# Performance work log

Hardware: AMD Instinct MI355X
Metric: run time of the kernel (lower is better)

## Reference

```python
import jax, jax.numpy as jnp
import numpy as np

N_SEQ, SEQ_LEN, HIDDEN, BATCH = 2048, 128, 128, 64


def setup_inputs() -> dict:
    key = jax.random.key(0)
    ks = jax.random.split(key, 6)
    s_ih = 1.0 / np.sqrt(SEQ_LEN)
    s_hh = 1.0 / np.sqrt(HIDDEN)
    s_fc = 1.0 / np.sqrt(N_SEQ * HIDDEN)
    return {
        "x": jax.random.normal(ks[0], (BATCH, N_SEQ, SEQ_LEN), dtype=jnp.float32),
        "h0": jnp.zeros((BATCH, HIDDEN), dtype=jnp.float32),
        "c0": jnp.zeros((BATCH, HIDDEN), dtype=jnp.float32),
        # LSTM weights, PyTorch gate order (i, f, g, o) packed on last axis
        "W_ih": jax.random.uniform(ks[1], (SEQ_LEN, 4 * HIDDEN), jnp.float32, -s_ih, s_ih),
        "W_hh": jax.random.uniform(ks[2], (HIDDEN, 4 * HIDDEN), jnp.float32, -s_hh, s_hh),
        "b": jax.random.uniform(ks[3], (4 * HIDDEN,), jnp.float32, -s_ih, s_ih),
        "fc_w": jax.random.uniform(ks[4], (2, N_SEQ * HIDDEN), jnp.float32, -s_fc, s_fc),
        "fc_b": jax.random.uniform(ks[5], (2,), jnp.float32, -s_fc, s_fc),
    }


def _lstm(x_tmajor, h0, c0, W_ih, W_hh, b):
    # x_tmajor: [T, B, D]. Precompute input projection in one big matmul.
    pre = jnp.einsum("tbd,dg->tbg", x_tmajor, W_ih) + b  # [T, B, 4H]
    H = h0.shape[-1]

    def step(carry, pre_t):
        h, c = carry
        gates = pre_t + h @ W_hh  # [B, 4H]
        i = jax.nn.sigmoid(gates[:, 0 * H:1 * H])
        f = jax.nn.sigmoid(gates[:, 1 * H:2 * H])
        g = jnp.tanh(gates[:, 2 * H:3 * H])
        o = jax.nn.sigmoid(gates[:, 3 * H:4 * H])
        c_new = f * c + i * g
        h_new = o * jnp.tanh(c_new)
        return (h_new, c_new), h_new

    (_, _), hs = jax.lax.scan(step, (h0, c0), pre)
    return hs  # [T, B, H]


def reference(x, h0, c0, W_ih, W_hh, b, fc_w, fc_b):
    xt = jnp.transpose(x, (1, 0, 2))              # [T, B, D]
    hs = _lstm(xt, h0, c0, W_ih, W_hh, b)          # [T, B, H]
    hb = jnp.transpose(hs, (1, 0, 2))              # [B, T, H]
    flat = hb.reshape(hb.shape[0], -1)             # [B, T*H]
    return flat @ fc_w.T + fc_b                    # [B, 2]
```

## Files before the change

### kernel.cpp

```cpp
#include <hip/hip_runtime.h>

#define T_SEQ 2048
#define NBATCH 64
#define DIM 128
#define HID 128
#define G4 512
#define GRP 16
#define TT 8
#define LOG2E 1.44269504088896f

typedef _Float16 h2v   __attribute__((ext_vector_type(2)));
typedef _Float16 f16x8 __attribute__((ext_vector_type(8)));
typedef float    f32x4 __attribute__((ext_vector_type(4)));

__device__ __forceinline__ unsigned pack2(float lo, float hi) {
    h2v v; v.x = (_Float16)lo; v.y = (_Float16)hi;
    return __builtin_bit_cast(unsigned, v);
}
__device__ __forceinline__ float dot2(unsigned a, unsigned b, float c) {
#if __has_builtin(__builtin_amdgcn_fdot2)
    return __builtin_amdgcn_fdot2(__builtin_bit_cast(h2v, a),
                                  __builtin_bit_cast(h2v, b), c, false);
#else
    h2v av = __builtin_bit_cast(h2v, a), bv = __builtin_bit_cast(h2v, b);
    c = fmaf((float)av.x, (float)bv.x, c);
    return fmaf((float)av.y, (float)bv.y, c);
#endif
}
__device__ __forceinline__ float rcp_(float x)  { return __builtin_amdgcn_rcpf(x); }
__device__ __forceinline__ float exp2_(float x) { return __builtin_amdgcn_exp2f(x); }
template <int CTRL>
__device__ __forceinline__ float qmov(float v) {
    int r = __builtin_amdgcn_mov_dpp(__builtin_bit_cast(int, v), CTRL, 0xF, 0xF, true);
    return __builtin_bit_cast(float, r);
}
#define QP_XOR1 0xB1
#define QP_XOR2 0x4E
#define QP_B0   0x00
#define QP_B1   0x55
#define QP_B2   0xAA
#define QP_B3   0xFF

__device__ __forceinline__ void barrier_lgkm() {
    asm volatile("s_waitcnt lgkmcnt(0)\n\ts_barrier" ::: "memory");
    __builtin_amdgcn_sched_barrier(0);
}

__global__ __launch_bounds__(256) void prep(
    const float* __restrict__ x, _Float16* __restrict__ x16)
{
    const size_t gtid   = (size_t)blockIdx.x * blockDim.x + threadIdx.x;
    const size_t stride = (size_t)gridDim.x * blockDim.x;
    const size_t n_x2 = (size_t)NBATCH * T_SEQ * DIM / 2;
    for (size_t i = gtid; i < n_x2; i += stride) {
        float2 v = reinterpret_cast<const float2*>(x)[i];
        h2v p; p.x = (_Float16)v.x; p.y = (_Float16)v.y;
        reinterpret_cast<h2v*>(x16)[i] = p;
    }
}

__global__ __launch_bounds__(512, 2) void pre_mfma(
    const _Float16* __restrict__ x16,
    const float* __restrict__ Wih,
    const float* __restrict__ bias,
    _Float16* __restrict__ pre,
    int t0)
{
    const int tid = threadIdx.x;
    const int w   = tid >> 6;
    const int l   = tid & 63;
    const int col = l & 15;
    const int hi  = l >> 4;
    const int bg  = blockIdx.x & 3;
    const int lt0 = (blockIdx.x >> 2) * TT;
    const int batch = bg * 16 + col;

    f16x8 aX[4][4];
    f32x4 bv[4];
    #pragma unroll
    for (int j = 0; j < 4; ++j) {
        const int chr  = 16 * (4 * w + j) + col;
        const int wcol = (chr & 3) * HID + (chr >> 2);
        const float sc = ((chr & 3) == 2) ? -2.0f * LOG2E : -LOG2E;
        #pragma unroll
        for (int ks = 0; ks < 4; ++ks) {
            f16x8 a;
            #pragma unroll
            for (int i = 0; i < 8; ++i) {
                int k = ks * 32 + hi * 8 + i;
                a[i] = (_Float16)(Wih[(size_t)k * G4 + wcol] * sc);
            }
            aX[j][ks] = a;
        }
        #pragma unroll
        for (int r = 0; r < 4; ++r) {
            const int ch = 16 * (4 * w + j) + 4 * hi + r;
            const float scr = ((ch & 3) == 2) ? -2.0f * LOG2E : -LOG2E;
            bv[j][r] = bias[(ch & 3) * HID + (ch >> 2)] * scr;
        }
    }

    const _Float16* xb_base = x16 + (size_t)batch * T_SEQ * DIM + hi * 8;

    for (int tt = 0; tt < TT; ++tt) {
        const int lt = lt0 + tt;
        const int t  = t0 + lt;
        f16x8 xf[4];
        #pragma unroll
        for (int ks = 0; ks < 4; ++ks)
            xf[ks] = *reinterpret_cast<const f16x8*>(
                xb_base + (size_t)t * DIM + ks * 32);
        #pragma unroll
        for (int j = 0; j < 4; ++j) {
            f32x4 acc = bv[j];
            #pragma unroll
            for (int ks = 0; ks < 4; ++ks)
                acc = __builtin_amdgcn_mfma_f32_16x16x32_f16(aX[j][ks], xf[ks], acc, 0, 0, 0);
            uint2 o;
            o.x = pack2(acc[0], acc[1]);
            o.y = pack2(acc[2], acc[3]);
            *reinterpret_cast<uint2*>(
                pre + ((size_t)lt * NBATCH + batch) * G4 + 16 * (4 * w + j) + 4 * hi) = o;
        }
    }
}

__global__ __launch_bounds__(512, 1) void lstm_scan(
    const _Float16* __restrict__ pre,
    const float* __restrict__ Whh,
    const float* __restrict__ h0,
    const float* __restrict__ c0,
    float* __restrict__ state,
    _Float16* __restrict__ trace,
    int t0, int tc)
{
    __shared__ __align__(16) _Float16 h_sh[2][HID];

    const int tid = threadIdx.x;
    const int j = tid >> 2;
    const int q = tid & 3;
    const int b = blockIdx.x;
    const bool q1 = (q & 1) != 0;
    const bool q2 = (q & 2) != 0;

    float* st_h = state;
    float* st_c = state + NBATCH * HID;

    unsigned wpk[4][16];
    #pragma unroll
    for (int g = 0; g < 4; ++g) {
        const float sc = (g == 2) ? -2.0f * LOG2E : -LOG2E;
        #pragma unroll
        for (int i = 0; i < 16; ++i) {
            int k0 = q * 32 + 2 * i;
            wpk[g][i] = pack2(Whh[(size_t)k0 * G4 + g * HID + j] * sc,
                              Whh[(size_t)(k0 + 1) * G4 + g * HID + j] * sc);
        }
    }

    float c, hj;
    if (t0 == 0) {
        hj = h0[b * HID + j]; c = c0[b * HID + j];
    } else {
        hj = st_h[b * HID + j];
        c  = st_c[b * HID + j];
    }
    if (q == 0) h_sh[0][j] = (_Float16)hj;

    const size_t pstep = (size_t)NBATCH * G4;
    const _Float16* pb = pre + (size_t)b * G4 + tid;
    _Float16* tb = trace + ((size_t)b * T_SEQ + t0) * HID + j;

    unsigned short prA[GRP], prB[GRP];
    #pragma unroll
    for (int s = 0; s < GRP; ++s)
        prA[s] = __builtin_bit_cast(unsigned short, pb[(size_t)s * pstep]);

    __syncthreads();

#define LOADG(PR, TGN)                                                       \
    {                                                                        \
        const int tgl = (TGN);                                               \
        _Pragma("unroll")                                                    \
        for (int s = 0; s < GRP; ++s)                                        \
            PR[s] = __builtin_bit_cast(unsigned short,                       \
                        pb[(size_t)(tgl + s) * pstep]);                      \
    }

#define STEP16(PR, TG)                                                       \
    _Pragma("unroll")                                                        \
    for (int s = 0; s < GRP; ++s) {                                          \
        const int cur = s & 1;                                               \
        const uint4* hp = reinterpret_cast<const uint4*>(&h_sh[cur][q * 32]);\
        float a0 = 0.f, a1 = 0.f, a2 = 0.f, a3 = 0.f;                        \
        _Pragma("unroll")                                                    \
        for (int m = 0; m < 4; ++m) {                                        \
            uint4 hv = hp[m];                                                \
            a0 = dot2(hv.x, wpk[0][4 * m + 0], a0);                          \
            a1 = dot2(hv.x, wpk[1][4 * m + 0], a1);                          \
            a2 = dot2(hv.x, wpk[2][4 * m + 0], a2);                          \
            a3 = dot2(hv.x, wpk[3][4 * m + 0], a3);                          \
            a0 = dot2(hv.y, wpk[0][4 * m + 1], a0);                          \
            a1 = dot2(hv.y, wpk[1][4 * m + 1], a1);                          \
            a2 = dot2(hv.y, wpk[2][4 * m + 1], a2);                          \
            a3 = dot2(hv.y, wpk[3][4 * m + 1], a3);                          \
            a0 = dot2(hv.z, wpk[0][4 * m + 2], a0);                          \
            a1 = dot2(hv.z, wpk[1][4 * m + 2], a1);                          \
            a2 = dot2(hv.z, wpk[2][4 * m + 2], a2);                          \
            a3 = dot2(hv.z, wpk[3][4 * m + 2], a3);                          \
            a0 = dot2(hv.w, wpk[0][4 * m + 3], a0);                          \
            a1 = dot2(hv.w, wpk[1][4 * m + 3], a1);                          \
            a2 = dot2(hv.w, wpk[2][4 * m + 3], a2);                          \
            a3 = dot2(hv.w, wpk[3][4 * m + 3], a3);                          \
        }                                                                    \
        float t01  = q1 ? a1 : a0;                                           \
        float t01o = q1 ? a0 : a1;                                           \
        t01 += qmov<QP_XOR1>(t01o);                                          \
        float t23  = q1 ? a3 : a2;                                           \
        float t23o = q1 ? a2 : a3;                                           \
        t23 += qmov<QP_XOR1>(t23o);                                          \
        float tq  = q2 ? t23 : t01;                                          \
        float tqo = q2 ? t01 : t23;                                          \
        tq += qmov<QP_XOR2>(tqo);                                            \
        tq += (float)__builtin_bit_cast(_Float16, PR[s]);                    \
        float v = rcp_(1.0f + exp2_(tq));                                    \
        float gi = qmov<QP_B0>(v);                                           \
        float gf = qmov<QP_B1>(v);                                           \
        float vg = qmov<QP_B2>(v);                                           \
        float go = qmov<QP_B3>(v);                                           \
        c = fmaf(gf, c, fmaf(gi + gi, vg, -gi));                             \
        float vc = rcp_(1.0f + exp2_(-2.0f * LOG2E * c));                    \
        float hn = fmaf(go + go, vc, -go);                                   \
        hj = hn;                                                             \
        _Float16 h16 = (_Float16)hn;                                         \
        if (q == 0) {                                                        \
            h_sh[cur ^ 1][j] = h16;                                          \
            tb[(size_t)((TG) + s) * HID] = h16;                              \
        }                                                                    \
        barrier_lgkm();                                                      \
    }

    for (int tg = 0; tg < tc; tg += 2 * GRP) {
        LOADG(prB, tg + GRP);
        STEP16(prA, tg);
        const int tga = (tg + 2 * GRP < tc) ? tg + 2 * GRP : tg;
        LOADG(prA, tga);
        STEP16(prB, tg + GRP);
    }
#undef LOADG
#undef STEP16

    if (t0 + tc < T_SEQ) {
        if (q == 0) { st_h[b * HID + j] = hj; st_c[b * HID + j] = c; }
    }
}

__global__ __launch_bounds__(256) void fc_head(
    const _Float16* __restrict__ trace,
    const float* __restrict__ fcw,
    const float* __restrict__ fcb,
    float* __restrict__ out)
{
    __shared__ float red[4][2];
    const int b = blockIdx.x, tid = threadIdx.x;
    const _Float16* tbase = trace + (size_t)b * (T_SEQ * HID);
    const float* w0 = fcw;
    const float* w1 = fcw + (size_t)T_SEQ * HID;

    float s0 = 0.f, s1 = 0.f;
    for (int i = tid * 8; i < T_SEQ * HID; i += 256 * 8) {
        uint4 tv = *reinterpret_cast<const uint4*>(tbase + i);
        float wa0[8], wa1[8];
        *reinterpret_cast<float4*>(&wa0[0]) = *reinterpret_cast<const float4*>(w0 + i);
        *reinterpret_cast<float4*>(&wa0[4]) = *reinterpret_cast<const float4*>(w0 + i + 4);
        *reinterpret_cast<float4*>(&wa1[0]) = *reinterpret_cast<const float4*>(w1 + i);
        *reinterpret_cast<float4*>(&wa1[4]) = *reinterpret_cast<const float4*>(w1 + i + 4);
        const unsigned* tw = reinterpret_cast<const unsigned*>(&tv);
        #pragma unroll
        for (int e = 0; e < 4; ++e) {
            h2v hh = __builtin_bit_cast(h2v, tw[e]);
            float hx = (float)hh.x, hy = (float)hh.y;
            s0 = fmaf(hx, wa0[2 * e], s0);
            s0 = fmaf(hy, wa0[2 * e + 1], s0);
            s1 = fmaf(hx, wa1[2 * e], s1);
            s1 = fmaf(hy, wa1[2 * e + 1], s1);
        }
    }
    #pragma unroll
    for (int d = 32; d >= 1; d >>= 1) {
        s0 += __shfl_xor(s0, d);
        s1 += __shfl_xor(s1, d);
    }
    const int w = tid >> 6;
    if ((tid & 63) == 0) { red[w][0] = s0; red[w][1] = s1; }
    __syncthreads();
    if (tid < 2) {
        float v = red[0][tid] + red[1][tid] + red[2][tid] + red[3][tid];
        out[b * 2 + tid] = v + fcb[tid];
    }
}

extern "C" void kernel_launch(void* const* d_in, const int* in_sizes, int n_in,
                              void* d_out, int out_size, void* d_ws, size_t ws_size,
                              hipStream_t stream) {
    const float* x    = (const float*)d_in[0];
    const float* h0   = (const float*)d_in[1];
    const float* c0   = (const float*)d_in[2];
    const float* Wih  = (const float*)d_in[3];
    const float* Whh  = (const float*)d_in[4];
    const float* bias = (const float*)d_in[5];
    const float* fcw  = (const float*)d_in[6];
    const float* fcb  = (const float*)d_in[7];
    float* out = (float*)d_out;

    char* wsb = (char*)d_ws;
    _Float16* x16   = (_Float16*)wsb;
    _Float16* trace = (_Float16*)(wsb + (size_t)NBATCH * T_SEQ * DIM * 2);
    float* state    = (float*)(wsb + 2 * (size_t)NBATCH * T_SEQ * DIM * 2);
    const size_t state_floats = (size_t)2 * NBATCH * HID;
    _Float16* pre = (_Float16*)(state + state_floats);

    const size_t head = 2 * (size_t)NBATCH * T_SEQ * DIM * 2 + state_floats * 4;
    const size_t per_t_bytes = (size_t)NBATCH * G4 * sizeof(_Float16);
    size_t avail = (ws_size > head) ? ws_size - head : 0;
    int Tc = (int)(avail / per_t_bytes);
    Tc &= ~(2 * GRP - 1);
    if (Tc < 2 * GRP) Tc = 2 * GRP;
    if (Tc > T_SEQ) Tc = T_SEQ;

    prep<<<512, 256, 0, stream>>>(x, x16);
    for (int t0 = 0; t0 < T_SEQ; t0 += Tc) {
        int tc = (t0 + Tc <= T_SEQ) ? Tc : (T_SEQ - t0);
        pre_mfma<<<(tc / TT) * 4, 512, 0, stream>>>(x16, Wih, bias, pre, t0);
        lstm_scan<<<64, 512, 0, stream>>>(pre, Whh, h0, c0, state, trace, t0, tc);
    }
    fc_head<<<64, 256, 0, stream>>>(trace, fcw, fcb, out);
}
```

Measured before the change: 1.162 ms.

## Prepack LSTM weights once in prep, double pre_mfma TT, split FC head

Moves the scaled fp16 packing of W_ih, W_hh and bias into the prep kernel, so pre_mfma and lstm_scan load prepacked coalesced arrays instead of doing strided gathers and conversions in every block. TT is doubled, which halves the pre_mfma grid and amortises weight loading over more timesteps. The FC head is split across 4 chunks per batch with a small final reduction kernel, to use more blocks. This adds workspace buffers and one extra launch.

```diff
diff --git a/kernel.cpp b/kernel.cpp
--- a/kernel.cpp
+++ b/kernel.cpp
@@ -6,7 +6,7 @@
 #define HID 128
 #define G4 512
 #define GRP 16
-#define TT 8
+#define TT 16
 #define LOG2E 1.44269504088896f
 
 typedef _Float16 h2v   __attribute__((ext_vector_type(2)));
@@ -47,22 +47,58 @@
 }
 
 __global__ __launch_bounds__(256) void prep(
-    const float* __restrict__ x, _Float16* __restrict__ x16)
+    const float* __restrict__ x,
+    const float* __restrict__ Wih,
+    const float* __restrict__ Whh,
+    const float* __restrict__ bias,
+    _Float16* __restrict__ x16,
+    _Float16* __restrict__ aXf,
+    unsigned* __restrict__ whh_pk,
+    float* __restrict__ bias_s)
 {
     const size_t gtid   = (size_t)blockIdx.x * blockDim.x + threadIdx.x;
     const size_t stride = (size_t)gridDim.x * blockDim.x;
+
     const size_t n_x2 = (size_t)NBATCH * T_SEQ * DIM / 2;
     for (size_t i = gtid; i < n_x2; i += stride) {
         float2 v = reinterpret_cast<const float2*>(x)[i];
         h2v p; p.x = (_Float16)v.x; p.y = (_Float16)v.y;
         reinterpret_cast<h2v*>(x16)[i] = p;
     }
+    for (size_t n = gtid; n < 65536; n += stride) {
+        int i  = (int)n & 7;
+        int l  = ((int)n >> 3) & 63;
+        int ks = ((int)n >> 9) & 3;
+        int j  = ((int)n >> 11) & 3;
+        int w  = (int)n >> 13;
+        int col = l & 15, hi = l >> 4;
+        int chr  = 16 * (4 * w + j) + col;
+        int wcol = (chr & 3) * HID + (chr >> 2);
+        float sc = ((chr & 3) == 2) ? -2.0f * LOG2E : -LOG2E;
+        int k = ks * 32 + hi * 8 + i;
+        aXf[n] = (_Float16)(Wih[(size_t)k * G4 + wcol] * sc);
+    }
+    for (size_t n = gtid; n < 32768; n += stride) {
+        int tid = (int)n & 511;
+        int gi  = (int)n >> 9;
+        int g = gi >> 4, ii = gi & 15;
+        int j = tid >> 2, q = tid & 3;
+        int k0 = q * 32 + 2 * ii;
+        float sc = (g == 2) ? -2.0f * LOG2E : -LOG2E;
+        whh_pk[n] = pack2(Whh[(size_t)k0 * G4 + g * HID + j] * sc,
+                          Whh[(size_t)(k0 + 1) * G4 + g * HID + j] * sc);
+    }
+    for (size_t n = gtid; n < 512; n += stride) {
+        int gate = (int)n & 3, u = (int)n >> 2;
+        float sc = (gate == 2) ? -2.0f * LOG2E : -LOG2E;
+        bias_s[n] = bias[gate * HID + u] * sc;
+    }
 }
 
 __global__ __launch_bounds__(512, 2) void pre_mfma(
     const _Float16* __restrict__ x16,
-    const float* __restrict__ Wih,
-    const float* __restrict__ bias,
+    const _Float16* __restrict__ aXf,
+    const float* __restrict__ bias_s,
     _Float16* __restrict__ pre,
     int t0)
 {
@@ -79,25 +115,11 @@
     f32x4 bv[4];
     #pragma unroll
     for (int j = 0; j < 4; ++j) {
-        const int chr  = 16 * (4 * w + j) + col;
-        const int wcol = (chr & 3) * HID + (chr >> 2);
-        const float sc = ((chr & 3) == 2) ? -2.0f * LOG2E : -LOG2E;
-        #pragma unroll
-        for (int ks = 0; ks < 4; ++ks) {
-            f16x8 a;
-            #pragma unroll
-            for (int i = 0; i < 8; ++i) {
-                int k = ks * 32 + hi * 8 + i;
-                a[i] = (_Float16)(Wih[(size_t)k * G4 + wcol] * sc);
-            }
-            aX[j][ks] = a;
-        }
-        #pragma unroll
-        for (int r = 0; r < 4; ++r) {
-            const int ch = 16 * (4 * w + j) + 4 * hi + r;
-            const float scr = ((ch & 3) == 2) ? -2.0f * LOG2E : -LOG2E;
-            bv[j][r] = bias[(ch & 3) * HID + (ch >> 2)] * scr;
-        }
+        #pragma unroll
+        for (int ks = 0; ks < 4; ++ks)
+            aX[j][ks] = *reinterpret_cast<const f16x8*>(
+                aXf + (((size_t)(w * 4 + j) * 4 + ks) << 9) + l * 8);
+        bv[j] = *reinterpret_cast<const f32x4*>(bias_s + 64 * w + 16 * j + 4 * hi);
     }
 
     const _Float16* xb_base = x16 + (size_t)batch * T_SEQ * DIM + hi * 8;
@@ -127,7 +149,7 @@
 
 __global__ __launch_bounds__(512, 1) void lstm_scan(
     const _Float16* __restrict__ pre,
-    const float* __restrict__ Whh,
+    const unsigned* __restrict__ whh_pk,
     const float* __restrict__ h0,
     const float* __restrict__ c0,
     float* __restrict__ state,
@@ -148,15 +170,10 @@
 
     unsigned wpk[4][16];
     #pragma unroll
-    for (int g = 0; g < 4; ++g) {
-        const float sc = (g == 2) ? -2.0f * LOG2E : -LOG2E;
-        #pragma unroll
-        for (int i = 0; i < 16; ++i) {
-            int k0 = q * 32 + 2 * i;
-            wpk[g][i] = pack2(Whh[(size_t)k0 * G4 + g * HID + j] * sc,
-                              Whh[(size_t)(k0 + 1) * G4 + g * HID + j] * sc);
-        }
-    }
+    for (int g = 0; g < 4; ++g)
+        #pragma unroll
+        for (int ii = 0; ii < 16; ++ii)
+            wpk[g][ii] = whh_pk[(size_t)(g * 16 + ii) * 512 + tid];
 
     float c, hj;
     if (t0 == 0) {
@@ -255,20 +272,21 @@
     }
 }
 
-__global__ __launch_bounds__(256) void fc_head(
+__global__ __launch_bounds__(256) void fc_part(
     const _Float16* __restrict__ trace,
     const float* __restrict__ fcw,
-    const float* __restrict__ fcb,
-    float* __restrict__ out)
+    float* __restrict__ part)
 {
     __shared__ float red[4][2];
-    const int b = blockIdx.x, tid = threadIdx.x;
-    const _Float16* tbase = trace + (size_t)b * (T_SEQ * HID);
-    const float* w0 = fcw;
-    const float* w1 = fcw + (size_t)T_SEQ * HID;
+    const int b = blockIdx.x, ck = blockIdx.y, tid = threadIdx.x;
+    const int n4 = T_SEQ * HID / 4;
+    const int base = ck * n4;
+    const _Float16* tbase = trace + (size_t)b * (T_SEQ * HID) + base;
+    const float* w0 = fcw + base;
+    const float* w1 = fcw + (size_t)T_SEQ * HID + base;
 
     float s0 = 0.f, s1 = 0.f;
-    for (int i = tid * 8; i < T_SEQ * HID; i += 256 * 8) {
+    for (int i = tid * 8; i < n4; i += 256 * 8) {
         uint4 tv = *reinterpret_cast<const uint4*>(tbase + i);
         float wa0[8], wa1[8];
         *reinterpret_cast<float4*>(&wa0[0]) = *reinterpret_cast<const float4*>(w0 + i);
@@ -295,9 +313,21 @@
     if ((tid & 63) == 0) { red[w][0] = s0; red[w][1] = s1; }
     __syncthreads();
     if (tid < 2) {
-        float v = red[0][tid] + red[1][tid] + red[2][tid] + red[3][tid];
-        out[b * 2 + tid] = v + fcb[tid];
-    }
+        part[(b * 4 + ck) * 2 + tid] =
+            red[0][tid] + red[1][tid] + red[2][tid] + red[3][tid];
+    }
+}
+
+__global__ __launch_bounds__(128) void fc_fin(
+    const float* __restrict__ part,
+    const float* __restrict__ fcb,
+    float* __restrict__ out)
+{
+    const int tid = threadIdx.x;
+    const int b = tid >> 1, o = tid & 1;
+    float v = part[(b * 4 + 0) * 2 + o] + part[(b * 4 + 1) * 2 + o]
+            + part[(b * 4 + 2) * 2 + o] + part[(b * 4 + 3) * 2 + o];
+    out[b * 2 + o] = v + fcb[o];
 }
 
 extern "C" void kernel_launch(void* const* d_in, const int* in_sizes, int n_in,
@@ -314,13 +344,17 @@
     float* out = (float*)d_out;
 
     char* wsb = (char*)d_ws;
-    _Float16* x16   = (_Float16*)wsb;
-    _Float16* trace = (_Float16*)(wsb + (size_t)NBATCH * T_SEQ * DIM * 2);
-    float* state    = (float*)(wsb + 2 * (size_t)NBATCH * T_SEQ * DIM * 2);
-    const size_t state_floats = (size_t)2 * NBATCH * HID;
-    _Float16* pre = (_Float16*)(state + state_floats);
-
-    const size_t head = 2 * (size_t)NBATCH * T_SEQ * DIM * 2 + state_floats * 4;
+    const size_t X = (size_t)NBATCH * T_SEQ * DIM * 2;
+    _Float16* x16    = (_Float16*)wsb;
+    _Float16* trace  = (_Float16*)(wsb + X);
+    float*    state  = (float*)(wsb + 2 * X);
+    float*    part   = (float*)(wsb + 2 * X + 65536);
+    _Float16* aXf    = (_Float16*)(wsb + 2 * X + 65536 + 2048);
+    unsigned* whh_pk = (unsigned*)(wsb + 2 * X + 65536 + 2048 + 131072);
+    float*    bias_s = (float*)(wsb + 2 * X + 65536 + 2048 + 2 * 131072);
+    _Float16* pre    = (_Float16*)(wsb + 2 * X + 65536 + 2048 + 2 * 131072 + 2048);
+
+    const size_t head = 2 * X + 65536 + 2048 + 2 * 131072 + 2048;
     const size_t per_t_bytes = (size_t)NBATCH * G4 * sizeof(_Float16);
     size_t avail = (ws_size > head) ? ws_size - head : 0;
     int Tc = (int)(avail / per_t_bytes);
@@ -328,11 +362,12 @@
     if (Tc < 2 * GRP) Tc = 2 * GRP;
     if (Tc > T_SEQ) Tc = T_SEQ;
 
-    prep<<<512, 256, 0, stream>>>(x, x16);
+    prep<<<512, 256, 0, stream>>>(x, Wih, Whh, bias, x16, aXf, whh_pk, bias_s);
     for (int t0 = 0; t0 < T_SEQ; t0 += Tc) {
         int tc = (t0 + Tc <= T_SEQ) ? Tc : (T_SEQ - t0);
-        pre_mfma<<<(tc / TT) * 4, 512, 0, stream>>>(x16, Wih, bias, pre, t0);
-        lstm_scan<<<64, 512, 0, stream>>>(pre, Whh, h0, c0, state, trace, t0, tc);
-    }
-    fc_head<<<64, 256, 0, stream>>>(trace, fcw, fcb, out);
-}
+        pre_mfma<<<(tc / TT) * 4, 512, 0, stream>>>(x16, aXf, bias_s, pre, t0);
+        lstm_scan<<<64, 512, 0, stream>>>(pre, whh_pk, h0, c0, state, trace, t0, tc);
+    }
+    fc_part<<<dim3(64, 4), 256, 0, stream>>>(trace, fcw, part);
+    fc_fin<<<1, 128, 0, stream>>>(part, fcb, out);
+}
```

New measurement: 1.076 ms (median of 2 runs). 1.08x faster.
